# Kernel optimization log

Measured on AMD Instinct MI355X. Metric: run time of the kernel, lower is better.

Reference implementation:

```python
import jax, jax.numpy as jnp
import numpy as np

B, C, T = 16, 768, 1024
STEPS, NNEG, OFFSET = 12, 10, 1
COPIES = NNEG + 1


def setup_inputs() -> dict:
    key = jax.random.key(0)
    k1, k2, k3, k4 = jax.random.split(key, 4)
    x = jax.random.normal(k1, (B, C, T), jnp.float32)
    y = jax.random.normal(k2, (B, C, T), jnp.float32)
    # ConvTranspose2d(in_dim, out_dim, (1, steps)) weight -> [C_in, C_out, steps]
    W = jax.random.normal(k3, (C, C, STEPS), jnp.float32) * 0.02
    b = jnp.zeros((C,), jnp.float32)
    # Negative-sample indices, replicating torch sample_negatives (sample_distance=None):
    # randint in [0, T-1), bump collisions with the positive timestep, add per-batch offset.
    neg = jax.random.randint(k4, (B, NNEG * T), 0, T - 1)
    tszs = jnp.repeat(jnp.arange(T), NNEG)  # [NNEG*T]
    neg = jnp.where(neg >= tszs[None, :], neg + 1, neg)
    neg = neg + jnp.arange(B)[:, None] * T  # index into flattened [B*T]
    return {"x": x, "y": y, "W": W, "b": b, "neg_idxs": neg}


def reference(x, y, W, b, neg_idxs):
    # project_to_steps: ConvTranspose2d with kernel (1, STEPS) on [B,C,T,1] -> [B,C,T,STEPS]
    proj = jnp.einsum('bct,cds->bdts', x, W) + b[None, :, None, None]

    # gather negatives: y -> [C, B*T], fancy-index, reshape to [NNEG, B, C, T]
    yf = jnp.transpose(y, (1, 0, 2)).reshape(C, B * T)
    negs = yf[:, neg_idxs.reshape(-1)].reshape(C, B, NNEG, T)
    negs = jnp.transpose(negs, (2, 1, 0, 3))  # [NNEG, B, C, T]

    targets = jnp.concatenate([y[None], negs], axis=0)  # [COPIES, B, C, T]

    steps = min(STEPS, T - OFFSET)
    preds = []
    for i in range(steps):  # small fixed loop over prediction steps (ragged slice sizes)
        off = i + OFFSET
        # [T-off, B, COPIES]: dot context at step i with targets shifted by off
        p = jnp.einsum('bct,nbct->tbn', proj[..., :T - off, i], targets[..., off:])
        preds.append(p.reshape(-1))
    predictions = jnp.concatenate(preds).reshape(-1, COPIES)  # infonce logits
    labels = jnp.zeros((predictions.shape[0],), jnp.int32)  # positive is copy 0
    return predictions, labels
```

## Files before the change

### kernel.cpp

```cpp
#include <hip/hip_runtime.h>

typedef __bf16 bf16;
typedef __attribute__((ext_vector_type(8))) __bf16 bf16x8;
typedef __attribute__((ext_vector_type(4))) __bf16 bf16x4;
typedef __attribute__((ext_vector_type(4))) float f32x4;

#define B_ 16
#define C_ 768
#define T_ 1024
#define S_ 12
#define NNEG_ 10
#define NCOPY 11
#define NPRED_ROWS 195360
#define NPRED (NPRED_ROWS * NCOPY)
#define NT_ 12

__device__ __forceinline__ void gload16(const void* g, void* l) {
    __builtin_amdgcn_global_load_lds(
        (__attribute__((address_space(1))) void*)g,
        (__attribute__((address_space(3))) void*)l, 16, 0, 0);
}

__global__ void k_wt(const float* __restrict__ W, bf16* __restrict__ WtT) {
    int id = blockIdx.x * blockDim.x + threadIdx.x;
    if (id >= C_ * C_) return;
    int d = id / C_, c = id % C_;
    const float* src = W + ((size_t)c * C_ + d) * S_;
#pragma unroll
    for (int s = 0; s < S_; ++s)
        WtT[(size_t)s * C_ * C_ + id] = (bf16)src[s];
}

__global__ void k_tr2(const float* __restrict__ x, const float* __restrict__ y,
                      bf16* __restrict__ xTc, bf16* __restrict__ yTc, int b0, int cb) {
    __shared__ float tile[32][33];
    int zz = blockIdx.z;
    const float* src = (zz < cb) ? x : y;
    bf16* dst = (zz < cb) ? xTc : yTc;
    int bb = (zz < cb) ? zz : zz - cb;
    int b = b0 + bb;
    int c0 = blockIdx.y * 32, t0 = blockIdx.x * 32;
    int tx = threadIdx.x & 31, ty = threadIdx.x >> 5;
#pragma unroll
    for (int i = 0; i < 4; ++i)
        tile[ty + i * 8][tx] = src[((size_t)b * C_ + c0 + ty + i * 8) * T_ + t0 + tx];
    __syncthreads();
#pragma unroll
    for (int i = 0; i < 4; ++i)
        dst[((size_t)bb * T_ + t0 + ty + i * 8) * C_ + c0 + tx] = (bf16)tile[tx][ty + i * 8];
}

#define SBAR()  __builtin_amdgcn_s_barrier()
#define SCHED() __builtin_amdgcn_sched_barrier(0)
#define LGKM0() asm volatile("s_waitcnt lgkmcnt(0)" ::: "memory")

__global__ __launch_bounds__(512, 2) void k_gemm8(
    const bf16* __restrict__ xTc, const bf16* __restrict__ WtT,
    const float* __restrict__ bias, bf16* __restrict__ P)
{
    const int q    = gridDim.x >> 3;
    const int orig = blockIdx.x;
    const int id2  = (orig & 7) * q + (orig >> 3);
    const int bb   = id2 / 144;
    const int rem  = id2 % 144;
    const int tblk = rem / 36;
    const int nblk = rem % 36;

    const int tid  = threadIdx.x;
    const int wv   = tid >> 6, lane = tid & 63;
    const int mwz  = wv >> 2, nwz = wv & 3;
    const int quad = lane >> 4, l15 = lane & 15;

    __shared__ __align__(16) bf16 sA[2][256][64];
    __shared__ __align__(16) bf16 sB[2][256][64];

    const int lrow = lane >> 3;
    const int laneOff = lrow * 1536 + (((lane & 7) * 16) ^ (lrow << 4));
    const char* aG = (const char*)(WtT + (size_t)(nblk * 256) * C_) + laneOff;
    const char* bG = (const char*)(xTc + ((size_t)bb * T_ + tblk * 256) * C_) + laneOff;
    const int h0 = wv * 16, h1 = wv * 16 + 8;
    const int arw0 = (h0 & 63) + ((h0 >> 6) << 7);
    const int arw1 = (h1 & 63) + ((h1 >> 6) << 7);
    const int brw0 = (h0 & 31) + ((h0 >> 5) << 6);
    const int brw1 = (h1 & 31) + ((h1 >> 5) << 6);

#define STAGE_A(bufn, roff, kt) do { \
    gload16(aG + (size_t)(arw0 + (roff)) * 1536 + (kt) * 128, &sA[bufn][arw0 + (roff)][0]); \
    gload16(aG + (size_t)(arw1 + (roff)) * 1536 + (kt) * 128, &sA[bufn][arw1 + (roff)][0]); \
} while (0)
#define STAGE_B(bufn, roff, kt) do { \
    gload16(bG + (size_t)(brw0 + (roff)) * 1536 + (kt) * 128, &sB[bufn][brw0 + (roff)][0]); \
    gload16(bG + (size_t)(brw1 + (roff)) * 1536 + (kt) * 128, &sB[bufn][brw1 + (roff)][0]); \
} while (0)

    const int csw0 = (quad * 16) ^ ((l15 & 7) << 4);
    const int csw1 = (64 + quad * 16) ^ ((l15 & 7) << 4);
    const char* aRd0 = (const char*)&sA[0][mwz * 128 + l15][0] + csw0;
    const char* aRd1 = (const char*)&sA[0][mwz * 128 + l15][0] + csw1;
    const char* bRd0 = (const char*)&sB[0][nwz * 64 + l15][0] + csw0;
    const char* bRd1 = (const char*)&sB[0][nwz * 64 + l15][0] + csw1;

    f32x4 acc[8][4] = {};

    STAGE_A(0, 0, 0);
    STAGE_A(0, 64, 0);
    STAGE_B(0, 32, 0);
    STAGE_B(0, 0, 0);
    STAGE_A(1, 0, 1);
    STAGE_B(1, 32, 1);
    STAGE_A(1, 64, 1);
    asm volatile("s_waitcnt vmcnt(6)" ::: "memory");
    SCHED(); SBAR(); SCHED();

#pragma unroll 2
    for (int j = 0; j < NT_; ++j) {
        const int cur = j & 1;
        const int coff = cur << 15;
        const char* aC0 = aRd0 + coff; const char* aC1 = aRd1 + coff;
        const char* bC0 = bRd0 + coff; const char* bC1 = bRd1 + coff;

        bf16x8 a03[4][2], a47[4][2], b01[2][2], b23[2][2], b01p[2][2];

        if (j + 1 < NT_) STAGE_B(cur ^ 1, 0, j + 1);
#pragma unroll
        for (int i = 0; i < 4; ++i) {
            a03[i][0] = *(const bf16x8*)(aC0 + i * 2048);
            a03[i][1] = *(const bf16x8*)(aC1 + i * 2048);
        }
#pragma unroll
        for (int i = 0; i < 2; ++i) {
            b01[i][0] = *(const bf16x8*)(bC0 + i * 2048);
            b01[i][1] = *(const bf16x8*)(bC1 + i * 2048);
        }
        SCHED(); SBAR(); LGKM0(); SCHED();
        __builtin_amdgcn_s_setprio(1);
#pragma unroll
        for (int i = 0; i < 4; ++i)
#pragma unroll
            for (int n = 0; n < 2; ++n)
#pragma unroll
                for (int kk = 0; kk < 2; ++kk)
                    acc[i][n] = __builtin_amdgcn_mfma_f32_16x16x32_bf16(a03[i][kk], b01[n][kk], acc[i][n], 0, 0, 0);
        __builtin_amdgcn_s_setprio(0);
        SCHED(); SBAR(); SCHED();

        if (j + 2 < NT_) STAGE_A(cur, 0, j + 2);
#pragma unroll
        for (int i = 0; i < 2; ++i) {
            b23[i][0] = *(const bf16x8*)(bC0 + 4096 + i * 2048);
            b23[i][1] = *(const bf16x8*)(bC1 + 4096 + i * 2048);
        }
        SCHED(); SBAR(); LGKM0(); SCHED();
        __builtin_amdgcn_s_setprio(1);
#pragma unroll
        for (int i = 0; i < 4; ++i)
#pragma unroll
            for (int n = 0; n < 2; ++n)
#pragma unroll
                for (int kk = 0; kk < 2; ++kk)
                    acc[i][2 + n] = __builtin_amdgcn_mfma_f32_16x16x32_bf16(a03[i][kk], b23[n][kk], acc[i][2 + n], 0, 0, 0);
        __builtin_amdgcn_s_setprio(0);
        SCHED(); SBAR(); SCHED();

        if (j + 2 < NT_) STAGE_B(cur, 32, j + 2);
#pragma unroll
        for (int i = 0; i < 4; ++i) {
            a47[i][0] = *(const bf16x8*)(aC0 + 8192 + i * 2048);
            a47[i][1] = *(const bf16x8*)(aC1 + 8192 + i * 2048);
        }
        SCHED(); SBAR(); LGKM0(); SCHED();
        __builtin_amdgcn_s_setprio(1);
#pragma unroll
        for (int i = 0; i < 4; ++i)
#pragma unroll
            for (int n = 0; n < 2; ++n)
#pragma unroll
                for (int kk = 0; kk < 2; ++kk)
                    acc[4 + i][2 + n] = __builtin_amdgcn_mfma_f32_16x16x32_bf16(a47[i][kk], b23[n][kk], acc[4 + i][2 + n], 0, 0, 0);
        __builtin_amdgcn_s_setprio(0);
        SCHED(); SBAR(); SCHED();

        if (j + 2 < NT_) STAGE_A(cur, 64, j + 2);
#pragma unroll
        for (int i = 0; i < 2; ++i) {
            b01p[i][0] = *(const bf16x8*)(bC0 + i * 2048);
            b01p[i][1] = *(const bf16x8*)(bC1 + i * 2048);
        }
        if (j < NT_ - 2)       { asm volatile("s_waitcnt vmcnt(6)" ::: "memory"); }
        else if (j == NT_ - 2) { asm volatile("s_waitcnt vmcnt(0)" ::: "memory"); }
        SCHED(); SBAR(); LGKM0(); SCHED();
        __builtin_amdgcn_s_setprio(1);
#pragma unroll
        for (int i = 0; i < 4; ++i)
#pragma unroll
            for (int n = 0; n < 2; ++n)
#pragma unroll
                for (int kk = 0; kk < 2; ++kk)
                    acc[4 + i][n] = __builtin_amdgcn_mfma_f32_16x16x32_bf16(a47[i][kk], b01p[n][kk], acc[4 + i][n], 0, 0, 0);
        __builtin_amdgcn_s_setprio(0);
        SCHED(); SBAR(); SCHED();
    }

    const size_t SC = (size_t)S_ * C_;
    bf16* Pb = P + ((size_t)bb * T_) * SC;
#pragma unroll
    for (int i = 0; i < 8; ++i) {
        const int nloc = mwz * 128 + i * 16 + quad * 4;
        const f32x4 bv = *(const f32x4*)&bias[(nblk % 3) * 256 + nloc];
#pragma unroll
        for (int n = 0; n < 4; ++n) {
            const int t = tblk * 256 + nwz * 64 + n * 16 + l15;
            bf16x4 v;
#pragma unroll
            for (int r = 0; r < 4; ++r) v[r] = (bf16)(acc[i][n][r] + bv[r]);
            *(bf16x4*)&Pb[(size_t)t * SC + nblk * 256 + nloc] = v;
        }
    }
#undef STAGE_A
#undef STAGE_B
}

__global__ __launch_bounds__(256) void k_pred(
    const bf16* __restrict__ P, const bf16* __restrict__ yTc,
    const int* __restrict__ neg, float* __restrict__ out, int b0)
{
    const int widx = (blockIdx.x << 2) + (threadIdx.x >> 6);
    const int lane = threadIdx.x & 63;
    const int bb = widx >> 10, tp = widx & 1023;
    const int b = b0 + bb;
    const int quad = lane >> 4, l15 = lane & 15;

    int sA = l15 < S_ ? l15 : S_ - 1;
    int tA = tp - 1 - sA;
    if (tA < 0) tA = 0;
    const bf16* arow = P + ((size_t)bb * T_ + tA) * (S_ * C_) + sA * C_ + quad * 8;

    int ridx;
    if (l15 == 0)            ridx = bb * T_ + tp;
    else if (l15 < NCOPY)    ridx = neg[(size_t)b * (NNEG_ * T_) + (l15 - 1) * T_ + tp] - b0 * T_;
    else                     ridx = bb * T_ + tp;
    const bf16* brow = yTc + (size_t)ridx * C_ + quad * 8;

    f32x4 acc = {};
#pragma unroll 4
    for (int kt = 0; kt < C_ / 32; ++kt) {
        bf16x8 av = *(const bf16x8*)(arow + kt * 32);
        bf16x8 bv = *(const bf16x8*)(brow + kt * 32);
        acc = __builtin_amdgcn_mfma_f32_16x16x32_bf16(av, bv, acc, 0, 0, 0);
    }

#pragma unroll
    for (int r = 0; r < 4; ++r) {
        int s = quad * 4 + r;
        int t = tp - 1 - s;
        if (s < S_ && t >= 0) {
            int rowbase = s * (T_ - 1) - (s * (s - 1)) / 2;
            size_t row = (size_t)(rowbase + t) * B_ + b;
            if (l15 < NCOPY)       out[row * NCOPY + l15] = acc[r];
            else if (l15 == NCOPY) out[NPRED + row] = 0.0f;
        }
    }
}

extern "C" void kernel_launch(void* const* d_in, const int* in_sizes, int n_in,
                              void* d_out, int out_size, void* d_ws, size_t ws_size,
                              hipStream_t stream) {
    const float* x    = (const float*)d_in[0];
    const float* y    = (const float*)d_in[1];
    const float* W    = (const float*)d_in[2];
    const float* bias = (const float*)d_in[3];
    const int*   neg  = (const int*)d_in[4];
    float* out = (float*)d_out;

    const size_t offW    = (size_t)S_ * C_ * C_ * 2;
    const size_t perb_xy = (size_t)T_ * C_ * 2;
    const size_t perb_p  = (size_t)T_ * S_ * C_ * 2;
    const size_t perb    = 2 * perb_xy + perb_p;

    int bchunk = (int)((ws_size - offW) / perb);
    if (bchunk < 1) bchunk = 1;
    if (bchunk > B_) bchunk = B_;

    char* ws = (char*)d_ws;
    bf16* WtT = (bf16*)ws;
    bf16* xTc = (bf16*)(ws + offW);
    bf16* yTc = (bf16*)(ws + offW + (size_t)bchunk * perb_xy);
    bf16* P   = (bf16*)(ws + offW + (size_t)bchunk * perb_xy * 2);

    k_wt<<<dim3((C_ * C_ + 255) / 256), 256, 0, stream>>>(W, WtT);

    for (int b0 = 0; b0 < B_;) {
        int cb = bchunk < (B_ - b0) ? bchunk : (B_ - b0);
        k_tr2<<<dim3(T_ / 32, C_ / 32, 2 * cb), 256, 0, stream>>>(x, y, xTc, yTc, b0, cb);
        k_gemm8<<<dim3(cb * 144), 512, 0, stream>>>(xTc, WtT, bias, P);
        k_pred<<<dim3(cb * 256), 256, 0, stream>>>(P, yTc, neg, out, b0);
        b0 += cb;
    }
}
```

Baseline: 643.8 us.

## Stage prediction rows through swizzled LDS and use 3D grid for GEMM

Each k_pred block now handles a single timestep. All 256 threads cooperatively load the 12 projection rows and 12 target rows into XOR-swizzled shared memory with coalesced 8-byte loads, then one wave runs the MFMA loop out of LDS. This is meant to replace the scattered per-lane 16-byte global loads with coalesced ones, at the cost of four times as many blocks, a barrier, and three of four waves sitting idle during compute. The GEMM launch also switches from the XCD-remapped 1D block index to a plain 3D grid, which drops the L2-locality remapping.

```diff
diff --git a/kernel.cpp b/kernel.cpp
--- a/kernel.cpp
+++ b/kernel.cpp
@@ -58,13 +58,9 @@
     const bf16* __restrict__ xTc, const bf16* __restrict__ WtT,
     const float* __restrict__ bias, bf16* __restrict__ P)
 {
-    const int q    = gridDim.x >> 3;
-    const int orig = blockIdx.x;
-    const int id2  = (orig & 7) * q + (orig >> 3);
-    const int bb   = id2 / 144;
-    const int rem  = id2 % 144;
-    const int tblk = rem / 36;
-    const int nblk = rem % 36;
+    const int nblk = blockIdx.x;
+    const int tblk = blockIdx.y;
+    const int bb   = blockIdx.z;
 
     const int tid  = threadIdx.x;
     const int wv   = tid >> 6, lane = tid & 63;
@@ -220,32 +216,55 @@
 #undef STAGE_B
 }
 
-__global__ __launch_bounds__(256) void k_pred(
+__global__ __launch_bounds__(256, 4) void k_pred(
     const bf16* __restrict__ P, const bf16* __restrict__ yTc,
     const int* __restrict__ neg, float* __restrict__ out, int b0)
 {
-    const int widx = (blockIdx.x << 2) + (threadIdx.x >> 6);
-    const int lane = threadIdx.x & 63;
+    const int widx = blockIdx.x;
     const int bb = widx >> 10, tp = widx & 1023;
     const int b = b0 + bb;
+    const int tid = threadIdx.x;
+
+    __shared__ __align__(16) char sAB[24 * 1536];
+
+#pragma unroll
+    for (int i = 0; i < 18; ++i) {
+        int idx = i * 256 + tid;
+        int row = idx / 192;
+        int off = (idx % 192) * 8;
+        const bf16* grow;
+        if (row < 12) {
+            int tA = tp - 1 - row; if (tA < 0) tA = 0;
+            grow = P + ((size_t)bb * T_ + tA) * (S_ * C_) + row * C_;
+        } else {
+            int n = row - 12;
+            int ridx;
+            if (n == 0 || n >= NCOPY) ridx = bb * T_ + tp;
+            else ridx = neg[(size_t)b * (NNEG_ * T_) + (n - 1) * T_ + tp] - b0 * T_;
+            grow = yTc + (size_t)ridx * C_;
+        }
+        uint2 v = *(const uint2*)((const char*)grow + off);
+        int sb = (((off >> 4) << 4) ^ ((row & 7) << 4)) | (off & 8);
+        *(uint2*)(&sAB[row * 1536 + sb]) = v;
+    }
+    __syncthreads();
+
+    if (tid >= 64) return;
+    const int lane = tid;
     const int quad = lane >> 4, l15 = lane & 15;
 
-    int sA = l15 < S_ ? l15 : S_ - 1;
-    int tA = tp - 1 - sA;
-    if (tA < 0) tA = 0;
-    const bf16* arow = P + ((size_t)bb * T_ + tA) * (S_ * C_) + sA * C_ + quad * 8;
-
-    int ridx;
-    if (l15 == 0)            ridx = bb * T_ + tp;
-    else if (l15 < NCOPY)    ridx = neg[(size_t)b * (NNEG_ * T_) + (l15 - 1) * T_ + tp] - b0 * T_;
-    else                     ridx = bb * T_ + tp;
-    const bf16* brow = yTc + (size_t)ridx * C_ + quad * 8;
+    const int ra = l15 < 12 ? l15 : 11;
+    const int rb = 12 + (l15 < 12 ? l15 : 11);
+    const char* pa = sAB + ra * 1536;
+    const char* pb = sAB + rb * 1536;
+    const int xa = (ra & 7) << 4, xb = (rb & 7) << 4;
 
     f32x4 acc = {};
-#pragma unroll 4
-    for (int kt = 0; kt < C_ / 32; ++kt) {
-        bf16x8 av = *(const bf16x8*)(arow + kt * 32);
-        bf16x8 bv = *(const bf16x8*)(brow + kt * 32);
+#pragma unroll
+    for (int kt = 0; kt < 24; ++kt) {
+        const int col = ((kt << 2) + quad) << 4;
+        bf16x8 av = *(const bf16x8*)(pa + (col ^ xa));
+        bf16x8 bv = *(const bf16x8*)(pb + (col ^ xb));
         acc = __builtin_amdgcn_mfma_f32_16x16x32_bf16(av, bv, acc, 0, 0, 0);
     }
 
@@ -292,8 +311,8 @@
     for (int b0 = 0; b0 < B_;) {
         int cb = bchunk < (B_ - b0) ? bchunk : (B_ - b0);
         k_tr2<<<dim3(T_ / 32, C_ / 32, 2 * cb), 256, 0, stream>>>(x, y, xTc, yTc, b0, cb);
-        k_gemm8<<<dim3(cb * 144), 512, 0, stream>>>(xTc, WtT, bias, P);
-        k_pred<<<dim3(cb * 256), 256, 0, stream>>>(P, yTc, neg, out, b0);
+        k_gemm8<<<dim3(36, 4, cb), 512, 0, stream>>>(xTc, WtT, bias, P);
+        k_pred<<<dim3(cb << 10), 256, 0, stream>>>(P, yTc, neg, out, b0);
         b0 += cb;
     }
 }
```

Result: no change. 653.3 us (+1.5%).
